# Kernel optimization log

Measured on AMD Instinct MI355X. Metric: run time of the kernel, lower is better.

The kernel has to match this reference:

```python
import jax, jax.numpy as jnp
import numpy as np

K = 1024
HEADS = 16

def setup_inputs() -> dict:
    key = jax.random.key(0)
    ks = jax.random.split(key, 5)
    scale = 0.02
    x = jax.random.normal(ks[0], (2, 2048, K), dtype=jnp.float32)
    Wq = jax.random.normal(ks[1], (K, K), dtype=jnp.float32) * scale
    Wk = jax.random.normal(ks[2], (K, K), dtype=jnp.float32) * scale
    Wv = jax.random.normal(ks[3], (K, K), dtype=jnp.float32) * scale
    Wo = jax.random.normal(ks[4], (K, K), dtype=jnp.float32) * scale
    bo = jnp.zeros((K,), dtype=jnp.float32)
    return {"x": x, "Wq": Wq, "Wk": Wk, "Wv": Wv, "Wo": Wo, "bo": bo}

def reference(x, Wq, Wk, Wv, Wo, bo):
    b, t, k = x.shape
    h = HEADS
    s = k // h
    # projections (torch Linear: x @ W.T; weights here stored as [out,in])
    q = (x @ Wq.T).reshape(b, t, h, s).transpose(0, 2, 1, 3)  # [b,h,t,s]
    kk = (x @ Wk.T).reshape(b, t, h, s).transpose(0, 2, 1, 3)
    v = (x @ Wv.T).reshape(b, t, h, s).transpose(0, 2, 1, 3)
    # NOTE: original scales by sqrt(k) (full model dim), not sqrt(head_dim)
    scores = jnp.einsum('bhts,bhus->bhtu', q, kk) / jnp.sqrt(jnp.float32(k))
    attn = jax.nn.softmax(scores, axis=-1)
    y = jnp.einsum('bhtu,bhus->bhts', attn, v)  # [b,h,t,s]
    y = y.transpose(0, 2, 1, 3).reshape(b, t, k)
    return y @ Wo.T + bo
```

## Files before the change

### kernel.cpp

```cpp
#include <hip/hip_runtime.h>
#include <hip/hip_fp16.h>

typedef _Float16 f16;
typedef __attribute__((ext_vector_type(4))) _Float16 f16x4;
typedef __attribute__((ext_vector_type(8))) _Float16 f16x8;
typedef __attribute__((ext_vector_type(4))) float f32x4;

__device__ __forceinline__ void gload_lds16(const void* g, void* l) {
  __builtin_amdgcn_global_load_lds(
      (const __attribute__((address_space(1))) unsigned*)g,
      (__attribute__((address_space(3))) unsigned*)l, 16, 0, 0);
}

__global__ __launch_bounds__(256) void cvt_kernel(
    const float* __restrict__ x, const float* __restrict__ wq,
    const float* __restrict__ wk, const float* __restrict__ wv,
    const float* __restrict__ wo, f16* __restrict__ xh, f16* __restrict__ wh) {
  const int gid = blockIdx.x * 256 + threadIdx.x;
  const int XV = (4 * 1024 * 1024) / 4;
  if (gid < XV) {
    float4 t = ((const float4*)x)[gid];
    f16x4 o = {(f16)t.x, (f16)t.y, (f16)t.z, (f16)t.w};
    *(f16x4*)&xh[(size_t)gid * 4] = o;
  } else {
    int widx = gid - XV;
    int plane = widx >> 18;
    int off = widx & ((1 << 18) - 1);
    const float* src = (plane == 0) ? wq : (plane == 1) ? wk : (plane == 2) ? wv : wo;
    float4 t = ((const float4*)src)[off];
    if (plane == 0) {
      const float QS = 0.045084547f;
      t.x *= QS; t.y *= QS; t.z *= QS; t.w *= QS;
    }
    f16x4 o = {(f16)t.x, (f16)t.y, (f16)t.z, (f16)t.w};
    *(f16x4*)&wh[(size_t)widx * 4] = o;
  }
}

__global__ __launch_bounds__(512, 2) void gemm256(
    const f16* __restrict__ A, const f16* __restrict__ B, f16* __restrict__ C,
    int K, int ldc) {
  __shared__ __align__(16) f16 As[2][256][64];
  __shared__ __align__(16) f16 Bs[2][256][64];
  const int m0 = blockIdx.y * 256, n0 = blockIdx.x * 256;
  const int t = threadIdx.x;
  const int w = t >> 6, l = t & 63, g = l >> 4, c = l & 15;
  const int wm = (w >> 2) * 128, wn = (w & 3) * 64;

  auto stage = [&](int buf, int kt) {
#pragma unroll
    for (int i = 0; i < 4; ++i) {
      int ci = i * 512 + t;
      int row = ci >> 3, c8 = ci & 7;
      gload_lds16(&A[(size_t)(m0 + row) * K + kt * 64 + c8 * 8],
                  (char*)&As[buf][0][0] + (i * 512 + w * 64) * 16);
      gload_lds16(&B[(size_t)(n0 + row) * K + kt * 64 + c8 * 8],
                  (char*)&Bs[buf][0][0] + (i * 512 + w * 64) * 16);
    }
  };

  f32x4 acc[8][4] = {};
  const int nkt = K >> 6;
  stage(0, 0);
  int cur = 0;
  for (int kt = 0; kt < nkt; ++kt) {
    if (kt + 1 < nkt) {
      stage(cur ^ 1, kt + 1);
      asm volatile("s_waitcnt vmcnt(8)" ::: "memory");
    } else {
      asm volatile("s_waitcnt vmcnt(0)" ::: "memory");
    }
    __builtin_amdgcn_s_barrier();
#pragma unroll
    for (int kc = 0; kc < 2; ++kc) {
      f16x8 af[8], bf[4];
#pragma unroll
      for (int mi = 0; mi < 8; ++mi)
        af[mi] = *(const f16x8*)&As[cur][wm + mi * 16 + c][(kc * 4 + g) * 8];
#pragma unroll
      for (int ni = 0; ni < 4; ++ni)
        bf[ni] = *(const f16x8*)&Bs[cur][wn + ni * 16 + c][(kc * 4 + g) * 8];
      __builtin_amdgcn_s_setprio(1);
#pragma unroll
      for (int mi = 0; mi < 8; ++mi)
#pragma unroll
        for (int ni = 0; ni < 4; ++ni)
          acc[mi][ni] = __builtin_amdgcn_mfma_f32_16x16x32_f16(af[mi], bf[ni], acc[mi][ni], 0, 0, 0);
      __builtin_amdgcn_s_setprio(0);
    }
    __builtin_amdgcn_s_barrier();
    cur ^= 1;
  }
#pragma unroll
  for (int mi = 0; mi < 8; ++mi) {
    int rowb = m0 + wm + mi * 16 + 4 * g;
#pragma unroll
    for (int ni = 0; ni < 4; ++ni) {
      int col = n0 + wn + ni * 16 + c;
#pragma unroll
      for (int r = 0; r < 4; ++r)
        C[(size_t)(rowb + r) * ldc + col] = (f16)acc[mi][ni][r];
    }
  }
}

__global__ __launch_bounds__(256) void gemm_bt(
    const f16* __restrict__ A, const f16* __restrict__ B, float* __restrict__ C,
    const float* __restrict__ bias, int K, int ldc) {
  __shared__ __align__(16) f16 As[2][128][64];
  __shared__ __align__(16) f16 Bs[2][128][64];
  const int m0 = blockIdx.y * 128, n0 = blockIdx.x * 128;
  const int t = threadIdx.x;
  const int w = t >> 6, l = t & 63, g = l >> 4, c = l & 15;
  const int wm = (w >> 1) * 64, wn = (w & 1) * 64;

  auto stage = [&](int buf, int kt) {
#pragma unroll
    for (int i = 0; i < 4; ++i) {
      int ci = i * 256 + t;
      int row = ci >> 3, c8 = ci & 7;
      gload_lds16(&A[(size_t)(m0 + row) * K + kt * 64 + c8 * 8],
                  (char*)&As[buf][0][0] + (i * 256 + w * 64) * 16);
      gload_lds16(&B[(size_t)(n0 + row) * K + kt * 64 + c8 * 8],
                  (char*)&Bs[buf][0][0] + (i * 256 + w * 64) * 16);
    }
  };

  f32x4 acc[4][4] = {};
  const int nkt = K >> 6;
  stage(0, 0);
  int cur = 0;
  for (int kt = 0; kt < nkt; ++kt) {
    if (kt + 1 < nkt) {
      stage(cur ^ 1, kt + 1);
      asm volatile("s_waitcnt vmcnt(8)" ::: "memory");
    } else {
      asm volatile("s_waitcnt vmcnt(0)" ::: "memory");
    }
    __builtin_amdgcn_s_barrier();
#pragma unroll
    for (int kc = 0; kc < 2; ++kc) {
      f16x8 af[4], bf[4];
#pragma unroll
      for (int mi = 0; mi < 4; ++mi)
        af[mi] = *(const f16x8*)&As[cur][wm + mi * 16 + c][(kc * 4 + g) * 8];
#pragma unroll
      for (int ni = 0; ni < 4; ++ni)
        bf[ni] = *(const f16x8*)&Bs[cur][wn + ni * 16 + c][(kc * 4 + g) * 8];
#pragma unroll
      for (int mi = 0; mi < 4; ++mi)
#pragma unroll
        for (int ni = 0; ni < 4; ++ni)
          acc[mi][ni] = __builtin_amdgcn_mfma_f32_16x16x32_f16(af[mi], bf[ni], acc[mi][ni], 0, 0, 0);
    }
    __builtin_amdgcn_s_barrier();
    cur ^= 1;
  }
#pragma unroll
  for (int mi = 0; mi < 4; ++mi) {
    int rowb = m0 + wm + mi * 16 + 4 * g;
#pragma unroll
    for (int ni = 0; ni < 4; ++ni) {
      int col = n0 + wn + ni * 16 + c;
#pragma unroll
      for (int r = 0; r < 4; ++r)
        C[(size_t)(rowb + r) * ldc + col] = acc[mi][ni][r] + bias[col];
    }
  }
}

__global__ __launch_bounds__(512, 4) void attn_kernel(const f16* __restrict__ qkv,
                                                      f16* __restrict__ yh) {
  __shared__ __align__(16) f16 Ks[2][2][64][64];
  __shared__ __align__(16) f16 Vt[2][2][64][64];
  const int t = threadIdx.x;
  const int w = t >> 6, l = t & 63, g = l >> 4, c = l & 15;
  const int half = w >> 2, wq = w & 3;
  const int bid = blockIdx.x;
  const int xcd = bid & 7, rest = bid >> 3;
  const int qc = rest & 15, bh = (rest >> 4) * 8 + xcd;
  const int b = bh >> 4, h = bh & 15;
  const int q0 = qc * 128 + wq * 32;
  const size_t LD = 3072;
  const f16* qp = qkv + (size_t)(b * 2048) * LD + h * 64;
  const f16* kp = qp + 1024;
  const f16* vp = qp + 2048;
  const int kbase = half * 1024;
  const int tg = t & 255;
  const int rp = tg & 31, vd0 = (tg >> 5) * 8;

  f16x8 qf[2][2];
#pragma unroll
  for (int rb = 0; rb < 2; ++rb)
#pragma unroll
    for (int kc = 0; kc < 2; ++kc)
      qf[rb][kc] = *(const f16x8*)&qp[(size_t)(q0 + rb * 16 + c) * LD + kc * 32 + g * 8];

  auto stageK = [&](int buf, int key0) {
#pragma unroll
    for (int i = 0; i < 2; ++i) {
      int ci = i * 256 + tg;
      int row = ci >> 3;
      int c8 = (ci & 7) ^ (row & 7);
      gload_lds16(&kp[(size_t)(key0 + row) * LD + c8 * 8],
                  (char*)&Ks[half][buf][0][0] + (i * 256 + wq * 64) * 16);
    }
  };
  auto writeV = [&](int buf, f16x8 xa, f16x8 xb) {
#pragma unroll
    for (int j = 0; j < 8; ++j) {
      int dd = vd0 + j;
      union { f16 h2[2]; unsigned u; } pk;
      pk.h2[0] = xa[j]; pk.h2[1] = xb[j];
      int off = dd * 128 + (((rp >> 2) ^ (dd & 7)) * 16) + 4 * (rp & 3);
      *(unsigned*)((char*)&Vt[half][buf][0][0] + off) = pk.u;
    }
  };

  f32x4 yacc[2][4] = {};
  float lr[2] = {0.f, 0.f};

  stageK(0, kbase);
  {
    f16x8 va = *(const f16x8*)&vp[(size_t)(kbase + 2 * rp) * LD + vd0];
    f16x8 vb = *(const f16x8*)&vp[(size_t)(kbase + 2 * rp + 1) * LD + vd0];
    writeV(0, va, vb);
  }
  __syncthreads();

  int cur = 0;
  for (int kt = 0; kt < 16; ++kt) {
    const bool hn = (kt < 15);
    f16x8 nva, nvb;
    if (hn) {
      int k0n = kbase + (kt + 1) * 64;
      stageK(cur ^ 1, k0n);
      nva = *(const f16x8*)&vp[(size_t)(k0n + 2 * rp) * LD + vd0];
      nvb = *(const f16x8*)&vp[(size_t)(k0n + 2 * rp + 1) * LD + vd0];
    }
    f32x4 s[2][4];
    __builtin_amdgcn_s_setprio(1);
#pragma unroll
    for (int kb = 0; kb < 4; ++kb) {
      int row = kb * 16 + c;
      f16x8 kf0 = *(const f16x8*)((char*)&Ks[half][cur][0][0] + row * 128 + ((g ^ (row & 7)) * 16));
      f16x8 kf1 = *(const f16x8*)((char*)&Ks[half][cur][0][0] + row * 128 + (((4 + g) ^ (row & 7)) * 16));
#pragma unroll
      for (int rb = 0; rb < 2; ++rb) {
        f32x4 acc = {};
        acc = __builtin_amdgcn_mfma_f32_16x16x32_f16(kf0, qf[rb][0], acc, 0, 0, 0);
        acc = __builtin_amdgcn_mfma_f32_16x16x32_f16(kf1, qf[rb][1], acc, 0, 0, 0);
        s[rb][kb] = acc;
      }
    }
    __builtin_amdgcn_s_setprio(0);
    f16x4 pf[2][4];
#pragma unroll
    for (int rb = 0; rb < 2; ++rb)
#pragma unroll
      for (int kb = 0; kb < 4; ++kb)
#pragma unroll
        for (int r = 0; r < 4; ++r) {
          float p = __builtin_amdgcn_exp2f(s[rb][kb][r]);
          lr[rb] += p;
          pf[rb][kb][r] = (f16)p;
        }
    __builtin_amdgcn_s_setprio(1);
#pragma unroll
    for (int kb = 0; kb < 4; ++kb)
#pragma unroll
      for (int sb = 0; sb < 4; ++sb) {
        int row = sb * 16 + c;
        f16x4 vf = *(const f16x4*)((char*)&Vt[half][cur][0][0] + row * 128 +
                                   (((2 * kb + (g >> 1)) ^ (row & 7)) * 16) + 8 * (g & 1));
        yacc[0][sb] = __builtin_amdgcn_mfma_f32_16x16x16f16(vf, pf[0][kb], yacc[0][sb], 0, 0, 0);
        yacc[1][sb] = __builtin_amdgcn_mfma_f32_16x16x16f16(vf, pf[1][kb], yacc[1][sb], 0, 0, 0);
      }
    __builtin_amdgcn_s_setprio(0);
    if (hn) writeV(cur ^ 1, nva, nvb);
    __syncthreads();
    cur ^= 1;
  }

  float* ys = (float*)&Ks[0][0][0][0];
  float* ls = (float*)&Vt[0][0][0][0];
  const int mbase = (wq * 64 + l) * 32;
  if (half == 1) {
#pragma unroll
    for (int rb = 0; rb < 2; ++rb) {
      ls[(wq * 64 + l) * 2 + rb] = lr[rb];
#pragma unroll
      for (int sb = 0; sb < 4; ++sb)
#pragma unroll
        for (int r = 0; r < 4; ++r)
          ys[mbase + rb * 16 + sb * 4 + r] = yacc[rb][sb][r];
    }
  }
  __syncthreads();
  if (half == 0) {
#pragma unroll
    for (int rb = 0; rb < 2; ++rb) {
      float lt = lr[rb] + ls[(wq * 64 + l) * 2 + rb];
      lt += __shfl_xor(lt, 16, 64);
      lt += __shfl_xor(lt, 32, 64);
      float inv = 1.f / lt;
#pragma unroll
      for (int sb = 0; sb < 4; ++sb) {
        f16x4 o;
#pragma unroll
        for (int r = 0; r < 4; ++r)
          o[r] = (f16)((yacc[rb][sb][r] + ys[mbase + rb * 16 + sb * 4 + r]) * inv);
        *(f16x4*)&yh[(size_t)(b * 2048 + q0 + rb * 16 + c) * 1024 + h * 64 + sb * 16 + 4 * g] = o;
      }
    }
  }
}

extern "C" void kernel_launch(void* const* d_in, const int* in_sizes, int n_in,
                              void* d_out, int out_size, void* d_ws, size_t ws_size,
                              hipStream_t stream) {
  (void)in_sizes; (void)n_in; (void)out_size; (void)ws_size;
  const float* x  = (const float*)d_in[0];
  const float* wq = (const float*)d_in[1];
  const float* wk = (const float*)d_in[2];
  const float* wv = (const float*)d_in[3];
  const float* wo = (const float*)d_in[4];
  const float* bo = (const float*)d_in[5];

  f16* xh   = (f16*)d_ws;
  f16* wh   = xh + (size_t)4096 * 1024;
  f16* qkvh = wh + (size_t)4 * 1024 * 1024;
  f16* yh   = qkvh + (size_t)4096 * 3072;
  float* out = (float*)d_out;

  cvt_kernel<<<8192, 256, 0, stream>>>(x, wq, wk, wv, wo, xh, wh);
  gemm256<<<dim3(12, 16), 512, 0, stream>>>(xh, wh, qkvh, 1024, 3072);
  attn_kernel<<<512, 512, 0, stream>>>(qkvh, yh);
  gemm_bt<<<dim3(8, 32), 256, 0, stream>>>(yh, wh + (size_t)3 * 1024 * 1024, out, bo, 1024, 1024);
}
```

Measured before the change: 228.1 us.

## Replace 256-tile QKV GEMM with templated 128-tile GEMM; transpose attention merge scratch

Removes the 256x256-tile, 512-thread QKV projection GEMM and runs it through the same 128x128-tile kernel as the output projection, now templated on epilogue (fp16 store vs fp32 plus bias). This raises the QKV grid from 192 to 768 blocks to fill all CUs, at the cost of lower per-block data reuse. The attention kernel's cross-half merge through LDS is also relaid out column-major by lane, to avoid bank conflicts on the scratch writes and reads.

```diff
diff --git a/kernel.cpp b/kernel.cpp
--- a/kernel.cpp
+++ b/kernel.cpp
@@ -37,75 +37,9 @@
   }
 }
 
-__global__ __launch_bounds__(512, 2) void gemm256(
-    const f16* __restrict__ A, const f16* __restrict__ B, f16* __restrict__ C,
-    int K, int ldc) {
-  __shared__ __align__(16) f16 As[2][256][64];
-  __shared__ __align__(16) f16 Bs[2][256][64];
-  const int m0 = blockIdx.y * 256, n0 = blockIdx.x * 256;
-  const int t = threadIdx.x;
-  const int w = t >> 6, l = t & 63, g = l >> 4, c = l & 15;
-  const int wm = (w >> 2) * 128, wn = (w & 3) * 64;
-
-  auto stage = [&](int buf, int kt) {
-#pragma unroll
-    for (int i = 0; i < 4; ++i) {
-      int ci = i * 512 + t;
-      int row = ci >> 3, c8 = ci & 7;
-      gload_lds16(&A[(size_t)(m0 + row) * K + kt * 64 + c8 * 8],
-                  (char*)&As[buf][0][0] + (i * 512 + w * 64) * 16);
-      gload_lds16(&B[(size_t)(n0 + row) * K + kt * 64 + c8 * 8],
-                  (char*)&Bs[buf][0][0] + (i * 512 + w * 64) * 16);
-    }
-  };
-
-  f32x4 acc[8][4] = {};
-  const int nkt = K >> 6;
-  stage(0, 0);
-  int cur = 0;
-  for (int kt = 0; kt < nkt; ++kt) {
-    if (kt + 1 < nkt) {
-      stage(cur ^ 1, kt + 1);
-      asm volatile("s_waitcnt vmcnt(8)" ::: "memory");
-    } else {
-      asm volatile("s_waitcnt vmcnt(0)" ::: "memory");
-    }
-    __builtin_amdgcn_s_barrier();
-#pragma unroll
-    for (int kc = 0; kc < 2; ++kc) {
-      f16x8 af[8], bf[4];
-#pragma unroll
-      for (int mi = 0; mi < 8; ++mi)
-        af[mi] = *(const f16x8*)&As[cur][wm + mi * 16 + c][(kc * 4 + g) * 8];
-#pragma unroll
-      for (int ni = 0; ni < 4; ++ni)
-        bf[ni] = *(const f16x8*)&Bs[cur][wn + ni * 16 + c][(kc * 4 + g) * 8];
-      __builtin_amdgcn_s_setprio(1);
-#pragma unroll
-      for (int mi = 0; mi < 8; ++mi)
-#pragma unroll
-        for (int ni = 0; ni < 4; ++ni)
-          acc[mi][ni] = __builtin_amdgcn_mfma_f32_16x16x32_f16(af[mi], bf[ni], acc[mi][ni], 0, 0, 0);
-      __builtin_amdgcn_s_setprio(0);
-    }
-    __builtin_amdgcn_s_barrier();
-    cur ^= 1;
-  }
-#pragma unroll
-  for (int mi = 0; mi < 8; ++mi) {
-    int rowb = m0 + wm + mi * 16 + 4 * g;
-#pragma unroll
-    for (int ni = 0; ni < 4; ++ni) {
-      int col = n0 + wn + ni * 16 + c;
-#pragma unroll
-      for (int r = 0; r < 4; ++r)
-        C[(size_t)(rowb + r) * ldc + col] = (f16)acc[mi][ni][r];
-    }
-  }
-}
-
-__global__ __launch_bounds__(256) void gemm_bt(
-    const f16* __restrict__ A, const f16* __restrict__ B, float* __restrict__ C,
+template <int EPI>
+__global__ __launch_bounds__(256) void gemm128(
+    const f16* __restrict__ A, const f16* __restrict__ B, void* __restrict__ Cv,
     const float* __restrict__ bias, int K, int ldc) {
   __shared__ __align__(16) f16 As[2][128][64];
   __shared__ __align__(16) f16 Bs[2][128][64];
@@ -163,8 +97,13 @@
     for (int ni = 0; ni < 4; ++ni) {
       int col = n0 + wn + ni * 16 + c;
 #pragma unroll
-      for (int r = 0; r < 4; ++r)
-        C[(size_t)(rowb + r) * ldc + col] = acc[mi][ni][r] + bias[col];
+      for (int r = 0; r < 4; ++r) {
+        if (EPI == 0) {
+          ((f16*)Cv)[(size_t)(rowb + r) * ldc + col] = (f16)acc[mi][ni][r];
+        } else {
+          ((float*)Cv)[(size_t)(rowb + r) * ldc + col] = acc[mi][ni][r] + bias[col];
+        }
+      }
     }
   }
 }
@@ -284,23 +223,23 @@
 
   float* ys = (float*)&Ks[0][0][0][0];
   float* ls = (float*)&Vt[0][0][0][0];
-  const int mbase = (wq * 64 + l) * 32;
+  const int col = wq * 64 + l;
   if (half == 1) {
 #pragma unroll
     for (int rb = 0; rb < 2; ++rb) {
-      ls[(wq * 64 + l) * 2 + rb] = lr[rb];
+      ls[rb * 256 + col] = lr[rb];
 #pragma unroll
       for (int sb = 0; sb < 4; ++sb)
 #pragma unroll
         for (int r = 0; r < 4; ++r)
-          ys[mbase + rb * 16 + sb * 4 + r] = yacc[rb][sb][r];
+          ys[(rb * 16 + sb * 4 + r) * 256 + col] = yacc[rb][sb][r];
     }
   }
   __syncthreads();
   if (half == 0) {
 #pragma unroll
     for (int rb = 0; rb < 2; ++rb) {
-      float lt = lr[rb] + ls[(wq * 64 + l) * 2 + rb];
+      float lt = lr[rb] + ls[rb * 256 + col];
       lt += __shfl_xor(lt, 16, 64);
       lt += __shfl_xor(lt, 32, 64);
       float inv = 1.f / lt;
@@ -309,7 +248,7 @@
         f16x4 o;
 #pragma unroll
         for (int r = 0; r < 4; ++r)
-          o[r] = (f16)((yacc[rb][sb][r] + ys[mbase + rb * 16 + sb * 4 + r]) * inv);
+          o[r] = (f16)((yacc[rb][sb][r] + ys[(rb * 16 + sb * 4 + r) * 256 + col]) * inv);
         *(f16x4*)&yh[(size_t)(b * 2048 + q0 + rb * 16 + c) * 1024 + h * 64 + sb * 16 + 4 * g] = o;
       }
     }
@@ -334,7 +273,7 @@
   float* out = (float*)d_out;
 
   cvt_kernel<<<8192, 256, 0, stream>>>(x, wq, wk, wv, wo, xh, wh);
-  gemm256<<<dim3(12, 16), 512, 0, stream>>>(xh, wh, qkvh, 1024, 3072);
+  gemm128<0><<<dim3(24, 32), 256, 0, stream>>>(xh, wh, qkvh, nullptr, 1024, 3072);
   attn_kernel<<<512, 512, 0, stream>>>(qkvh, yh);
-  gemm_bt<<<dim3(8, 32), 256, 0, stream>>>(yh, wh + (size_t)3 * 1024 * 1024, out, bo, 1024, 1024);
-}
+  gemm128<1><<<dim3(8, 32), 256, 0, stream>>>(yh, wh + (size_t)3 * 1024 * 1024, out, bo, 1024, 1024);
+}
```

After: 224.9 us. No clear change (-1.4%).
